# Performance work log

Measured on AMD Instinct MI355X. Metric: run time of the kernel, lower is better.

## Reference

```python
import jax, jax.numpy as jnp
import numpy as np

N_NODES = 50000


def _add_self_loops(src, dst, n):
    loop = jnp.arange(n, dtype=src.dtype)
    return jnp.concatenate([src, loop]), jnp.concatenate([dst, loop])


def gcn_conv(x, src, dst, W, b, n):
    # PyG GCNConv: out = D^-1/2 (A+I) D^-1/2 (x W) + b
    h = x @ W                                        # [N, out]
    deg = jnp.zeros((n,), h.dtype).at[dst].add(1.0)  # in-degree incl. self-loops
    dinv = jax.lax.rsqrt(jnp.maximum(deg, 1e-12))
    norm = dinv[src] * dinv[dst]                     # [E]
    msg = h[src] * norm[:, None]                     # [E, out] gather
    return jax.ops.segment_sum(msg, dst, num_segments=n) + b


def setup_inputs() -> dict:
    key = jax.random.key(0)
    ks = jax.random.split(key, 10)
    num_features, hidden = 256, 64
    x = jax.random.normal(ks[0], (N_NODES, num_features), jnp.float32)
    edge_index = jax.random.randint(ks[1], (2, 1600000), 0, N_NODES, jnp.int64)

    def glorot(k, fi, fo):
        s = jnp.sqrt(6.0 / (fi + fo)).astype(jnp.float32)
        return jax.random.uniform(k, (fi, fo), jnp.float32, -s, s)

    dims = [(num_features, 2 * hidden), (2 * hidden, hidden),
            (hidden, 2 * hidden), (2 * hidden, num_features)]
    params = {}
    for i, (fi, fo) in enumerate(dims):
        params[f"W{i+1}"] = glorot(ks[2 + i], fi, fo)
        params[f"b{i+1}"] = jnp.zeros((fo,), jnp.float32)
    return {"x": x, "edge_index": edge_index, **params}


def reference(x, edge_index, W1, b1, W2, b2, W3, b3, W4, b4):
    n = x.shape[0]
    src, dst = _add_self_loops(edge_index[0], edge_index[1], n)
    h = jax.nn.relu(gcn_conv(x, src, dst, W1, b1, n))
    z = jax.nn.relu(gcn_conv(h, src, dst, W2, b2, n))
    h = jax.nn.relu(gcn_conv(z, src, dst, W3, b3, n))
    x_hat = gcn_conv(h, src, dst, W4, b4, n)
    return x_hat
```

## Files before the change

### kernel.cpp

```cpp
#include <hip/hip_runtime.h>
#include <cstdint>
#include <cstddef>


static inline int cdiv(int a, int b) { return (a + b - 1) / b; }

typedef _Float16 half8v __attribute__((ext_vector_type(8)));
typedef float f32x4 __attribute__((ext_vector_type(4)));

#define NBMAX 784
#define SCHUNK 8192
#define NBH 256
#define NPW 320

__global__ __launch_bounds__(256) void k_prep_hist(
    const float* __restrict__ W1, const float* __restrict__ W2,
    const float* __restrict__ W3, const float* __restrict__ W4,
    _Float16* __restrict__ W1t, _Float16* __restrict__ W2t,
    _Float16* __restrict__ W3t, _Float16* __restrict__ W4t,
    const float* __restrict__ x, _Float16* __restrict__ bufX,
    const int* __restrict__ dst, int* __restrict__ bh, int* __restrict__ done,
    int* __restrict__ boff, int* __restrict__ bcur,
    int E, int nb, int perBlock) {
  int b = blockIdx.x;
  int tid = threadIdx.x;
  if (b >= NBH + NPW) {
    int t = (b - NBH - NPW) * 256 + tid;
    const float* ap = &x[(size_t)t * 8];
    float4 f0 = *(const float4*)ap;
    float4 f1 = *(const float4*)(ap + 4);
    half8v v;
    v[0] = (_Float16)f0.x; v[1] = (_Float16)f0.y;
    v[2] = (_Float16)f0.z; v[3] = (_Float16)f0.w;
    v[4] = (_Float16)f1.x; v[5] = (_Float16)f1.y;
    v[6] = (_Float16)f1.z; v[7] = (_Float16)f1.w;
    *(half8v*)&bufX[(size_t)t * 8] = v;
    return;
  }
  if (b >= NBH) {
    int t = (b - NBH) * 256 + tid;
    if (t < 32768) {
      int m = t >> 8, k = t & 255;
      W1t[t] = (_Float16)W1[k * 128 + m];
    } else if (t < 40960) {
      int u = t - 32768;
      int m = u >> 7, k = u & 127;
      W2t[u] = (_Float16)W2[k * 64 + m];
    } else if (t < 49152) {
      int u = t - 40960;
      int m = u >> 6, k = u & 63;
      W3t[u] = (_Float16)W3[k * 128 + m];
    } else if (t < 81920) {
      int u = t - 49152;
      int m = u >> 7, k = u & 127;
      W4t[u] = (_Float16)W4[k * 256 + m];
    }
    return;
  }
  __shared__ int h[NBMAX];
  __shared__ int tsum[256];
  __shared__ int amLast;
  for (int i = tid; i < nb; i += 256) h[i] = 0;
  __syncthreads();
  int beg = b * perBlock;
  int end = min(beg + perBlock, E);
  for (int e = beg + tid; e < end; e += 256)
    atomicAdd(&h[dst[e] >> 6], 1);
  __syncthreads();
  for (int i = tid; i < nb; i += 256)
    if (h[i]) atomicAdd(&bh[i], h[i]);
  __threadfence();
  __syncthreads();
  if (tid == 0) amLast = (atomicAdd(done, 1) == NBH - 1) ? 1 : 0;
  __syncthreads();
  if (!amLast) return;
  int v[4];
  int s = 0;
#pragma unroll
  for (int i = 0; i < 4; ++i) {
    int idx = tid * 4 + i;
    v[i] = (idx < nb) ? atomicAdd(&bh[idx], 0) : 0;
    s += v[i];
  }
  tsum[tid] = s;
  __syncthreads();
  int x2 = s;
  for (int d = 1; d < 256; d <<= 1) {
    int add = (tid >= d) ? tsum[tid - d] : 0;
    __syncthreads();
    x2 += add;
    tsum[tid] = x2;
    __syncthreads();
  }
  int base = x2 - s;
#pragma unroll
  for (int i = 0; i < 4; ++i) {
    int idx = tid * 4 + i;
    if (idx < nb) { boff[idx] = base; bcur[idx] = base; }
    base += v[i];
  }
  if (tid == 255) boff[nb] = base;
}

__device__ __forceinline__ void scatter_body(int* hist, int* base,
                                             const int* __restrict__ src,
                                             const int* __restrict__ dst,
                                             int* __restrict__ bcur,
                                             unsigned* __restrict__ tmp,
                                             int E, int nb, int b, int tid) {
  int beg = b * SCHUNK;
  int end = min(beg + SCHUNK, E);
  for (int i = tid; i < nb; i += 256) hist[i] = 0;
  __syncthreads();
  for (int e = beg + tid; e < end; e += 256)
    atomicAdd(&hist[dst[e] >> 6], 1);
  __syncthreads();
  for (int bb = tid; bb < nb; bb += 256) {
    int c = hist[bb];
    base[bb] = c ? atomicAdd(&bcur[bb], c) : 0;
    hist[bb] = 0;
  }
  __syncthreads();
  for (int e = beg + tid; e < end; e += 256) {
    int d = dst[e];
    int bb = d >> 6;
    int lp = atomicAdd(&hist[bb], 1);
    tmp[base[bb] + lp] = ((unsigned)(d & 63) << 16) | (unsigned)src[e];
  }
}

template <int M, int K, int BIAS, int RELU, int SCALE, int AF32, int OUTF16>
__device__ __forceinline__ void gemm_body(_Float16* Als,
                                          const void* __restrict__ Av,
                                          const _Float16* __restrict__ Wt,
                                          const float* __restrict__ bias,
                                          const float* __restrict__ dinv,
                                          void* __restrict__ Cv, int N,
                                          int bx, int tid) {
  const int NT = M / 64;
  const int ST = K / 32;
  const int ROWW = K + 8;
  const int r0 = bx * 64;

  const int CH = K / 8;
  for (int i = tid; i < 64 * CH; i += 256) {
    int r = i / CH, c = i % CH;
    int gr = r0 + r;
    if (gr >= N) gr = N - 1;
    half8v v;
    if (AF32) {
      const float* ap = &((const float*)Av)[(size_t)gr * K + c * 8];
      float4 f0 = *(const float4*)ap;
      float4 f1 = *(const float4*)(ap + 4);
      v[0] = (_Float16)f0.x; v[1] = (_Float16)f0.y;
      v[2] = (_Float16)f0.z; v[3] = (_Float16)f0.w;
      v[4] = (_Float16)f1.x; v[5] = (_Float16)f1.y;
      v[6] = (_Float16)f1.z; v[7] = (_Float16)f1.w;
    } else {
      v = *(const half8v*)&((const _Float16*)Av)[(size_t)gr * K + c * 8];
    }
    *(half8v*)&Als[r * ROWW + c * 8] = v;
  }

  const int w  = tid >> 6;
  const int l  = tid & 63;
  const int lr = l & 15;
  const int lk = l >> 4;

  half8v b_all[ST][NT];
#pragma unroll
  for (int s = 0; s < ST; ++s)
#pragma unroll
    for (int ct = 0; ct < NT; ++ct) {
      int col0 = (w * NT + ct) * 16;
      b_all[s][ct] = *(const half8v*)&Wt[(size_t)(col0 + lr) * K + s * 32 + lk * 8];
    }

  __syncthreads();

  for (int rt = 0; rt < 4; ++rt) {
    f32x4 acc[NT] = {};
#pragma unroll
    for (int s = 0; s < ST; ++s) {
      half8v a = *(const half8v*)&Als[(rt * 16 + lr) * ROWW + s * 32 + lk * 8];
#pragma unroll
      for (int ct = 0; ct < NT; ++ct)
        acc[ct] = __builtin_amdgcn_mfma_f32_16x16x32_f16(a, b_all[s][ct], acc[ct], 0, 0, 0);
    }
    int rbase = r0 + rt * 16;
    float dvv[4];
    int okr[4];
#pragma unroll
    for (int r = 0; r < 4; ++r) {
      int ro = rbase + lk * 4 + r;
      okr[r] = (ro < N);
      dvv[r] = (SCALE && okr[r]) ? dinv[ro] : 1.0f;
    }
#pragma unroll
    for (int ct = 0; ct < NT; ++ct) {
      int col = (w * NT + ct) * 16 + lr;
      float bs = BIAS ? bias[col] : 0.f;
#pragma unroll
      for (int r = 0; r < 4; ++r) {
        if (!okr[r]) continue;
        int ro = rbase + lk * 4 + r;
        float v = acc[ct][r] + bs;
        if (RELU) v = fmaxf(v, 0.f);
        if (SCALE) v *= dvv[r];
        if (OUTF16) {
          ((_Float16*)Cv)[(size_t)ro * M + col] = (_Float16)v;
        } else {
          __builtin_nontemporal_store(v, &((float*)Cv)[(size_t)ro * M + col]);
        }
      }
    }
  }
}

template <int M, int K, int BIAS, int RELU, int SCALE, int AF32, int OUTF16>
__global__ __launch_bounds__(256) void k_gemm_mfma(const void* __restrict__ Av,
                                                   const _Float16* __restrict__ Wt,
                                                   const float* __restrict__ bias,
                                                   const float* __restrict__ dinv,
                                                   void* __restrict__ Cv, int N) {
  __shared__ __align__(16) _Float16 Als[64 * (K + 8)];
  gemm_body<M, K, BIAS, RELU, SCALE, AF32, OUTF16>(Als, Av, Wt, bias, dinv, Cv, N,
                                                   blockIdx.x, threadIdx.x);
}

__global__ __launch_bounds__(256) void k_scat_gemm1(const int* __restrict__ src,
                                                    const int* __restrict__ dst,
                                                    int* __restrict__ bcur,
                                                    unsigned* __restrict__ tmp,
                                                    int E, int nb, int nsb,
                                                    const _Float16* __restrict__ bufX,
                                                    const _Float16* __restrict__ W1t,
                                                    _Float16* __restrict__ bufA, int N) {
  __shared__ __align__(16) _Float16 lds[64 * 264];
  int b = blockIdx.x;
  if (b < nsb) {
    int* hist = (int*)lds;
    int* base = hist + NBMAX;
    scatter_body(hist, base, src, dst, bcur, tmp, E, nb, b, threadIdx.x);
  } else {
    gemm_body<128, 256, 0, 0, 0, 0, 1>(lds, bufX, W1t, nullptr, nullptr, bufA, N,
                                       b - nsb, threadIdx.x);
  }
}

__global__ __launch_bounds__(256) void k_bsort(const unsigned* __restrict__ tmp,
                                               const int* __restrict__ boff,
                                               unsigned short* __restrict__ esrc,
                                               int* __restrict__ offs,
                                               int* __restrict__ counts,
                                               float* __restrict__ dinv,
                                               int N) {
  __shared__ int hist[64], cur[64];
  int b = blockIdx.x;
  int t = threadIdx.x;
  if (t < 64) hist[t] = 0;
  __syncthreads();
  int beg = boff[b], end = boff[b + 1];
  int cnt = end - beg;
  for (int i = t; i < cnt; i += 256) atomicAdd(&hist[tmp[beg + i] >> 16], 1);
  __syncthreads();
  if (t < 64) {
    int v = hist[t];
    int x = v;
#pragma unroll
    for (int d = 1; d < 64; d <<= 1) {
      int up = __shfl_up(x, d, 64);
      if (t >= d) x += up;
    }
    int ex = x - v;
    cur[t] = ex;
    int node = b * 64 + t;
    if (node < N) {
      counts[node] = v;
      offs[node] = beg + ex;
      dinv[node] = rsqrtf((float)(v + 1));
    }
  }
  __syncthreads();
  for (int i = t; i < cnt; i += 256) {
    unsigned v = tmp[beg + i];
    int pos = atomicAdd(&cur[v >> 16], 1);
    esrc[beg + pos] = (unsigned short)(v & 0xFFFFu);
  }
}

template <int W, int BIAS, int RELU, int POST, int ESCALE>
__global__ __launch_bounds__(256) void k_pull16(const _Float16* __restrict__ h,
                                                const unsigned short* __restrict__ esrc,
                                                const int* __restrict__ offs,
                                                const int* __restrict__ counts,
                                                const float* __restrict__ dinv,
                                                const float* __restrict__ bias,
                                                _Float16* __restrict__ out, int n) {
  const int LPR = W / 8;
  const int GRP = 64 / LPR;
  int node = blockIdx.x * 4 + (threadIdx.x >> 6);
  if (node >= n) return;
  int lane = threadIdx.x & 63;
  int g  = lane / LPR;
  int fl = lane % LPR;
  size_t rbase = (size_t)node * W + fl * 8;
  float dvn = dinv[node];

  float acc[8] = {};
  if (g == 0) {
    half8v sv = *(const half8v*)&h[rbase];
    float sc = ESCALE ? dvn : 1.0f;
#pragma unroll
    for (int q = 0; q < 8; ++q) acc[q] = sc * (float)sv[q];
  }

  int beg = offs[node];
  int cnt = counts[node];
  int j = g;
  for (; j + 3 * GRP < cnt; j += 4 * GRP) {
    int s0 = esrc[beg + j];
    int s1 = esrc[beg + j + GRP];
    int s2 = esrc[beg + j + 2 * GRP];
    int s3 = esrc[beg + j + 3 * GRP];
    half8v v0 = *(const half8v*)&h[(size_t)s0 * W + fl * 8];
    half8v v1 = *(const half8v*)&h[(size_t)s1 * W + fl * 8];
    half8v v2 = *(const half8v*)&h[(size_t)s2 * W + fl * 8];
    half8v v3 = *(const half8v*)&h[(size_t)s3 * W + fl * 8];
    if (ESCALE) {
      float d0 = dinv[s0], d1 = dinv[s1], d2 = dinv[s2], d3 = dinv[s3];
#pragma unroll
      for (int q = 0; q < 8; ++q)
        acc[q] += (d0 * (float)v0[q] + d1 * (float)v1[q]) +
                  (d2 * (float)v2[q] + d3 * (float)v3[q]);
    } else {
#pragma unroll
      for (int q = 0; q < 8; ++q)
        acc[q] += ((float)v0[q] + (float)v1[q]) + ((float)v2[q] + (float)v3[q]);
    }
  }
  for (; j < cnt; j += GRP) {
    int s = esrc[beg + j];
    half8v v = *(const half8v*)&h[(size_t)s * W + fl * 8];
    float ds = ESCALE ? dinv[s] : 1.0f;
#pragma unroll
    for (int q = 0; q < 8; ++q) acc[q] += ds * (float)v[q];
  }

#pragma unroll
  for (int d = LPR; d < 64; d <<= 1) {
#pragma unroll
    for (int q = 0; q < 8; ++q) acc[q] += __shfl_xor(acc[q], d, 64);
  }

  if (g == 0) {
    float t[8];
#pragma unroll
    for (int q = 0; q < 8; ++q) t[q] = dvn * acc[q];
    if (BIAS) {
#pragma unroll
      for (int q = 0; q < 8; ++q) t[q] += bias[fl * 8 + q];
    }
    if (RELU) {
#pragma unroll
      for (int q = 0; q < 8; ++q) t[q] = fmaxf(t[q], 0.f);
    }
    if (POST) {
#pragma unroll
      for (int q = 0; q < 8; ++q) t[q] *= dvn;
    }
    half8v o;
#pragma unroll
    for (int q = 0; q < 8; ++q) o[q] = (_Float16)t[q];
    *(half8v*)&out[rbase] = o;
  }
}

extern "C" void kernel_launch(void* const* d_in, const int* in_sizes, int n_in,
                              void* d_out, int out_size, void* d_ws, size_t ws_size,
                              hipStream_t stream) {
  const float* x  = (const float*)d_in[0];
  const int*   ei = (const int*)d_in[1];
  const float* W1 = (const float*)d_in[2];
  const float* b1 = (const float*)d_in[3];
  const float* W2 = (const float*)d_in[4];
  const float* b2 = (const float*)d_in[5];
  const float* W3 = (const float*)d_in[6];
  const float* b3 = (const float*)d_in[7];
  const float* W4 = (const float*)d_in[8];
  const float* b4 = (const float*)d_in[9];

  const int N = in_sizes[0] / 256;
  const int E = in_sizes[1] / 2;
  const int* src = ei;
  const int* dst = ei + E;
  const int nb = cdiv(N, 64);
  const int nsb = cdiv(E, SCHUNK);
  const int ncast = N * 256 / 2048;

  const int NP = 50176;
  int*   bh     = (int*)d_ws;
  int*   done   = bh + NBMAX;
  int*   boff   = bh + NBMAX + 16;
  int*   bcur   = boff + NBMAX;
  int*   counts = bcur + NBMAX;
  int*   offs   = counts + NP;
  float* dinv   = (float*)(offs + NP);
  unsigned short* esrc = (unsigned short*)(dinv + NP);
  _Float16* W1t = (_Float16*)(esrc + E);
  _Float16* W2t = W1t + 32768;
  _Float16* W3t = W2t + 8192;
  _Float16* W4t = W3t + 8192;
  unsigned* tmp = (unsigned*)(((uintptr_t)(W4t + 32768) + 255) & ~(uintptr_t)255);
  _Float16* bufA = (_Float16*)(((uintptr_t)(tmp + E) + 255) & ~(uintptr_t)255);
  _Float16* bufB = bufA + (size_t)N * 128;
  _Float16* bufC = bufB + (size_t)N * 128;
  _Float16* bufD = bufC + (size_t)N * 64;
  _Float16* bufX = bufB;
  float* out = (float*)d_out;

  dim3 blk(256);

  (void)hipMemsetAsync(bh, 0, (NBMAX + 16) * sizeof(int), stream);

  k_prep_hist<<<NBH + NPW + ncast, blk, 0, stream>>>(W1, W2, W3, W4,
                                                     W1t, W2t, W3t, W4t,
                                                     x, bufX,
                                                     dst, bh, done, boff, bcur,
                                                     E, nb, cdiv(E, NBH));
  k_scat_gemm1<<<nsb + cdiv(N, 64), blk, 0, stream>>>(src, dst, bcur, tmp, E, nb, nsb,
                                                      bufX, W1t, bufA, N);
  k_bsort<<<nb, blk, 0, stream>>>(tmp, boff, esrc, offs, counts, dinv, N);

  dim3 gpull(cdiv(N, 4));
  dim3 ggemm(cdiv(N, 64));

  k_pull16<128, 1, 1, 0, 1><<<gpull, blk, 0, stream>>>(bufA, esrc, offs, counts, dinv, b1, bufB, N);
  k_gemm_mfma<64, 128, 0, 0, 1, 0, 1><<<ggemm, blk, 0, stream>>>(bufB, W2t, nullptr, dinv, bufC, N);
  k_pull16<64, 1, 1, 1, 0><<<gpull, blk, 0, stream>>>(bufC, esrc, offs, counts, dinv, b2, bufD, N);
  k_pull16<64, 0, 0, 0, 0><<<gpull, blk, 0, stream>>>(bufD, esrc, offs, counts, dinv, nullptr, bufC, N);
  k_gemm_mfma<128, 64, 1, 1, 1, 0, 1><<<ggemm, blk, 0, stream>>>(bufC, W3t, b3, dinv, bufA, N);
  k_pull16<128, 0, 0, 0, 0><<<gpull, blk, 0, stream>>>(bufA, esrc, offs, counts, dinv, nullptr, bufB, N);
  k_gemm_mfma<256, 128, 1, 0, 0, 0, 0><<<ggemm, blk, 0, stream>>>(bufB, W4t, b4, nullptr, out, N);
}
```

Baseline: 293.2 us.

## Use coarser 256-node buckets with LDS-staged scatter and separate first GEMM

The edge bucketing now uses 256-node buckets (196 instead of 782), and the scatter kernel stages each chunk's edges in LDS, sorted by bucket, before writing them to global memory in contiguous runs. The per-bucket sort now scans over 256 bins with a block-wide scan, and the first GEMM is split out of the fused scatter+GEMM kernel into its own launch. The aim is fewer global atomics and more coalesced scatter writes, at the cost of larger per-bucket sorts, an extra launch, and no longer overlapping GEMM1 with the scatter.

```diff
diff --git a/kernel.cpp b/kernel.cpp
--- a/kernel.cpp
+++ b/kernel.cpp
@@ -8,7 +8,8 @@
 typedef _Float16 half8v __attribute__((ext_vector_type(8)));
 typedef float f32x4 __attribute__((ext_vector_type(4)));
 
-#define NBMAX 784
+#define NCB 200
+#define CBS 8
 #define SCHUNK 8192
 #define NBH 256
 #define NPW 320
@@ -57,7 +58,7 @@
     }
     return;
   }
-  __shared__ int h[NBMAX];
+  __shared__ int h[NCB];
   __shared__ int tsum[256];
   __shared__ int amLast;
   for (int i = tid; i < nb; i += 256) h[i] = 0;
@@ -65,7 +66,7 @@
   int beg = b * perBlock;
   int end = min(beg + perBlock, E);
   for (int e = beg + tid; e < end; e += 256)
-    atomicAdd(&h[dst[e] >> 6], 1);
+    atomicAdd(&h[dst[e] >> CBS], 1);
   __syncthreads();
   for (int i = tid; i < nb; i += 256)
     if (h[i]) atomicAdd(&bh[i], h[i]);
@@ -74,17 +75,10 @@
   if (tid == 0) amLast = (atomicAdd(done, 1) == NBH - 1) ? 1 : 0;
   __syncthreads();
   if (!amLast) return;
-  int v[4];
-  int s = 0;
-#pragma unroll
-  for (int i = 0; i < 4; ++i) {
-    int idx = tid * 4 + i;
-    v[i] = (idx < nb) ? atomicAdd(&bh[idx], 0) : 0;
-    s += v[i];
-  }
-  tsum[tid] = s;
-  __syncthreads();
-  int x2 = s;
+  int v = (tid < nb) ? atomicAdd(&bh[tid], 0) : 0;
+  tsum[tid] = v;
+  __syncthreads();
+  int x2 = v;
   for (int d = 1; d < 256; d <<= 1) {
     int add = (tid >= d) ? tsum[tid - d] : 0;
     __syncthreads();
@@ -92,55 +86,117 @@
     tsum[tid] = x2;
     __syncthreads();
   }
-  int base = x2 - s;
-#pragma unroll
-  for (int i = 0; i < 4; ++i) {
-    int idx = tid * 4 + i;
-    if (idx < nb) { boff[idx] = base; bcur[idx] = base; }
-    base += v[i];
-  }
-  if (tid == 255) boff[nb] = base;
-}
-
-__device__ __forceinline__ void scatter_body(int* hist, int* base,
-                                             const int* __restrict__ src,
-                                             const int* __restrict__ dst,
-                                             int* __restrict__ bcur,
-                                             unsigned* __restrict__ tmp,
-                                             int E, int nb, int b, int tid) {
+  if (tid < nb) { boff[tid] = x2 - v; bcur[tid] = x2 - v; }
+  if (tid == nb - 1) boff[nb] = x2;
+}
+
+__global__ __launch_bounds__(256) void k_bscatter(const int* __restrict__ src,
+                                                  const int* __restrict__ dst,
+                                                  int* __restrict__ bcur,
+                                                  unsigned* __restrict__ tmp,
+                                                  int E, int nb) {
+  __shared__ unsigned stage[SCHUNK];
+  __shared__ int hist[NCB], lofs[NCB], gbase[NCB];
+  __shared__ int tsum[256];
+  int b = blockIdx.x;
+  int tid = threadIdx.x;
   int beg = b * SCHUNK;
   int end = min(beg + SCHUNK, E);
+  int cnt = end - beg;
   for (int i = tid; i < nb; i += 256) hist[i] = 0;
   __syncthreads();
   for (int e = beg + tid; e < end; e += 256)
-    atomicAdd(&hist[dst[e] >> 6], 1);
-  __syncthreads();
-  for (int bb = tid; bb < nb; bb += 256) {
-    int c = hist[bb];
-    base[bb] = c ? atomicAdd(&bcur[bb], c) : 0;
-    hist[bb] = 0;
+    atomicAdd(&hist[dst[e] >> CBS], 1);
+  __syncthreads();
+  int v = (tid < nb) ? hist[tid] : 0;
+  tsum[tid] = v;
+  __syncthreads();
+  int x = v;
+  for (int d = 1; d < 256; d <<= 1) {
+    int add = (tid >= d) ? tsum[tid - d] : 0;
+    __syncthreads();
+    x += add;
+    tsum[tid] = x;
+    __syncthreads();
+  }
+  if (tid < nb) {
+    int ex = x - v;
+    lofs[tid] = ex;
+    gbase[tid] = v ? atomicAdd(&bcur[tid], v) : 0;
+    hist[tid] = ex;
   }
   __syncthreads();
   for (int e = beg + tid; e < end; e += 256) {
     int d = dst[e];
-    int bb = d >> 6;
-    int lp = atomicAdd(&hist[bb], 1);
-    tmp[base[bb] + lp] = ((unsigned)(d & 63) << 16) | (unsigned)src[e];
+    int bb = d >> CBS;
+    int p = atomicAdd(&hist[bb], 1);
+    stage[p] = ((unsigned)d << 16) | (unsigned)src[e];
+  }
+  __syncthreads();
+  for (int i = tid; i < cnt; i += 256) {
+    unsigned v2 = stage[i];
+    int bb = v2 >> (16 + CBS);
+    tmp[gbase[bb] + (i - lofs[bb])] = v2;
+  }
+}
+
+__global__ __launch_bounds__(256) void k_bsort(const unsigned* __restrict__ tmp,
+                                               const int* __restrict__ boff,
+                                               unsigned short* __restrict__ esrc,
+                                               int* __restrict__ offs,
+                                               int* __restrict__ counts,
+                                               float* __restrict__ dinv,
+                                               int N) {
+  __shared__ int hist[256], cur[256], tsum[256];
+  int b = blockIdx.x;
+  int t = threadIdx.x;
+  hist[t] = 0;
+  __syncthreads();
+  int beg = boff[b], end = boff[b + 1];
+  int cnt = end - beg;
+  for (int i = t; i < cnt; i += 256)
+    atomicAdd(&hist[(tmp[beg + i] >> 16) & 255], 1);
+  __syncthreads();
+  int v = hist[t];
+  tsum[t] = v;
+  __syncthreads();
+  int x = v;
+  for (int d = 1; d < 256; d <<= 1) {
+    int add = (t >= d) ? tsum[t - d] : 0;
+    __syncthreads();
+    x += add;
+    tsum[t] = x;
+    __syncthreads();
+  }
+  int ex = x - v;
+  cur[t] = ex;
+  int node = b * 256 + t;
+  if (node < N) {
+    counts[node] = v;
+    offs[node] = beg + ex;
+    dinv[node] = rsqrtf((float)(v + 1));
+  }
+  __syncthreads();
+  for (int i = t; i < cnt; i += 256) {
+    unsigned v2 = tmp[beg + i];
+    int bin = (v2 >> 16) & 255;
+    int pos = atomicAdd(&cur[bin], 1);
+    esrc[beg + pos] = (unsigned short)(v2 & 0xFFFFu);
   }
 }
 
 template <int M, int K, int BIAS, int RELU, int SCALE, int AF32, int OUTF16>
-__device__ __forceinline__ void gemm_body(_Float16* Als,
-                                          const void* __restrict__ Av,
-                                          const _Float16* __restrict__ Wt,
-                                          const float* __restrict__ bias,
-                                          const float* __restrict__ dinv,
-                                          void* __restrict__ Cv, int N,
-                                          int bx, int tid) {
+__global__ __launch_bounds__(256) void k_gemm_mfma(const void* __restrict__ Av,
+                                                   const _Float16* __restrict__ Wt,
+                                                   const float* __restrict__ bias,
+                                                   const float* __restrict__ dinv,
+                                                   void* __restrict__ Cv, int N) {
   const int NT = M / 64;
   const int ST = K / 32;
   const int ROWW = K + 8;
-  const int r0 = bx * 64;
+  __shared__ __align__(16) _Float16 Als[64 * (K + 8)];
+  const int tid = threadIdx.x;
+  const int r0 = blockIdx.x * 64;
 
   const int CH = K / 8;
   for (int i = tid; i < 64 * CH; i += 256) {
@@ -214,78 +270,6 @@
         }
       }
     }
-  }
-}
-
-template <int M, int K, int BIAS, int RELU, int SCALE, int AF32, int OUTF16>
-__global__ __launch_bounds__(256) void k_gemm_mfma(const void* __restrict__ Av,
-                                                   const _Float16* __restrict__ Wt,
-                                                   const float* __restrict__ bias,
-                                                   const float* __restrict__ dinv,
-                                                   void* __restrict__ Cv, int N) {
-  __shared__ __align__(16) _Float16 Als[64 * (K + 8)];
-  gemm_body<M, K, BIAS, RELU, SCALE, AF32, OUTF16>(Als, Av, Wt, bias, dinv, Cv, N,
-                                                   blockIdx.x, threadIdx.x);
-}
-
-__global__ __launch_bounds__(256) void k_scat_gemm1(const int* __restrict__ src,
-                                                    const int* __restrict__ dst,
-                                                    int* __restrict__ bcur,
-                                                    unsigned* __restrict__ tmp,
-                                                    int E, int nb, int nsb,
-                                                    const _Float16* __restrict__ bufX,
-                                                    const _Float16* __restrict__ W1t,
-                                                    _Float16* __restrict__ bufA, int N) {
-  __shared__ __align__(16) _Float16 lds[64 * 264];
-  int b = blockIdx.x;
-  if (b < nsb) {
-    int* hist = (int*)lds;
-    int* base = hist + NBMAX;
-    scatter_body(hist, base, src, dst, bcur, tmp, E, nb, b, threadIdx.x);
-  } else {
-    gemm_body<128, 256, 0, 0, 0, 0, 1>(lds, bufX, W1t, nullptr, nullptr, bufA, N,
-                                       b - nsb, threadIdx.x);
-  }
-}
-
-__global__ __launch_bounds__(256) void k_bsort(const unsigned* __restrict__ tmp,
-                                               const int* __restrict__ boff,
-                                               unsigned short* __restrict__ esrc,
-                                               int* __restrict__ offs,
-                                               int* __restrict__ counts,
-                                               float* __restrict__ dinv,
-                                               int N) {
-  __shared__ int hist[64], cur[64];
-  int b = blockIdx.x;
-  int t = threadIdx.x;
-  if (t < 64) hist[t] = 0;
-  __syncthreads();
-  int beg = boff[b], end = boff[b + 1];
-  int cnt = end - beg;
-  for (int i = t; i < cnt; i += 256) atomicAdd(&hist[tmp[beg + i] >> 16], 1);
-  __syncthreads();
-  if (t < 64) {
-    int v = hist[t];
-    int x = v;
-#pragma unroll
-    for (int d = 1; d < 64; d <<= 1) {
-      int up = __shfl_up(x, d, 64);
-      if (t >= d) x += up;
-    }
-    int ex = x - v;
-    cur[t] = ex;
-    int node = b * 64 + t;
-    if (node < N) {
-      counts[node] = v;
-      offs[node] = beg + ex;
-      dinv[node] = rsqrtf((float)(v + 1));
-    }
-  }
-  __syncthreads();
-  for (int i = t; i < cnt; i += 256) {
-    unsigned v = tmp[beg + i];
-    int pos = atomicAdd(&cur[v >> 16], 1);
-    esrc[beg + pos] = (unsigned short)(v & 0xFFFFu);
   }
 }
 
@@ -394,16 +378,16 @@
   const int E = in_sizes[1] / 2;
   const int* src = ei;
   const int* dst = ei + E;
-  const int nb = cdiv(N, 64);
+  const int nb = cdiv(N, 256);
   const int nsb = cdiv(E, SCHUNK);
   const int ncast = N * 256 / 2048;
 
   const int NP = 50176;
   int*   bh     = (int*)d_ws;
-  int*   done   = bh + NBMAX;
-  int*   boff   = bh + NBMAX + 16;
-  int*   bcur   = boff + NBMAX;
-  int*   counts = bcur + NBMAX;
+  int*   done   = bh + NCB;
+  int*   boff   = bh + NCB + 16;
+  int*   bcur   = boff + NCB;
+  int*   counts = bcur + NCB;
   int*   offs   = counts + NP;
   float* dinv   = (float*)(offs + NP);
   unsigned short* esrc = (unsigned short*)(dinv + NP);
@@ -421,16 +405,16 @@
 
   dim3 blk(256);
 
-  (void)hipMemsetAsync(bh, 0, (NBMAX + 16) * sizeof(int), stream);
+  (void)hipMemsetAsync(bh, 0, (NCB + 16) * sizeof(int), stream);
 
   k_prep_hist<<<NBH + NPW + ncast, blk, 0, stream>>>(W1, W2, W3, W4,
                                                      W1t, W2t, W3t, W4t,
                                                      x, bufX,
                                                      dst, bh, done, boff, bcur,
                                                      E, nb, cdiv(E, NBH));
-  k_scat_gemm1<<<nsb + cdiv(N, 64), blk, 0, stream>>>(src, dst, bcur, tmp, E, nb, nsb,
-                                                      bufX, W1t, bufA, N);
+  k_bscatter<<<nsb, blk, 0, stream>>>(src, dst, bcur, tmp, E, nb);
   k_bsort<<<nb, blk, 0, stream>>>(tmp, boff, esrc, offs, counts, dinv, N);
+  k_gemm_mfma<128, 256, 0, 0, 0, 0, 1><<<cdiv(N, 64), blk, 0, stream>>>(bufX, W1t, nullptr, nullptr, bufA, N);
 
   dim3 gpull(cdiv(N, 4));
   dim3 ggemm(cdiv(N, 64));
```

Measured after the change: 306.7 us. +4.6%, slower.
